# Performance work log

Measured on AMD Instinct MI355X. Metric: run time of the kernel, lower is better.

The kernel has to match this reference:

```python
import jax, jax.numpy as jnp
from jax import lax
import numpy as np

B, T, IN, H, C, L = 128, 80, 4096, 512, 32000, 10


def setup_inputs() -> dict:
    key = jax.random.key(0)
    ks = jax.random.split(key, 19)
    s = 0.05  # param scale for numerical stability
    f = lambda k, shape: (jax.random.normal(k, shape, jnp.float32) * s)
    return {
        "data": jax.random.normal(ks[0], (B, T, IN), jnp.float32),
        "target": jax.random.randint(ks[1], (B, L), 0, C),
        "enc_lin_w": f(ks[2], (H, IN)),
        "enc_lin_b": f(ks[3], (H,)),
        "enc_wih0": f(ks[4], (2, 3 * H, H)),
        "enc_whh0": f(ks[5], (2, 3 * H, H)),
        "enc_bih0": f(ks[6], (2, 3 * H)),
        "enc_bhh0": f(ks[7], (2, 3 * H)),
        "enc_wih1": f(ks[8], (2, 3 * H, 2 * H)),
        "enc_whh1": f(ks[9], (2, 3 * H, H)),
        "enc_bih1": f(ks[10], (2, 3 * H)),
        "enc_bhh1": f(ks[11], (2, 3 * H)),
        "dec_wih": f(ks[12], (3 * H, H)),
        "dec_whh": f(ks[13], (3 * H, H)),
        "dec_bih": f(ks[14], (3 * H,)),
        "dec_bhh": f(ks[15], (3 * H,)),
        "out_w": f(ks[16], (C, 2 * H)),
        "out_b": f(ks[17], (C,)),
        "embed": f(ks[18], (C, H)),
    }


def _gru_cell(x, h, wih, whh, bih, bhh):
    # PyTorch GRU gate math, gates stacked (r, z, n) along 3H.
    gi = x @ wih.T + bih  # (B, 3H)
    gh = h @ whh.T + bhh
    ir, iz, inn = jnp.split(gi, 3, axis=-1)
    hr, hz, hn = jnp.split(gh, 3, axis=-1)
    r = jax.nn.sigmoid(ir + hr)
    z = jax.nn.sigmoid(iz + hz)
    n = jnp.tanh(inn + r * hn)
    return (1.0 - z) * n + z * h


def _gru_layer(x, wih, whh, bih, bhh, reverse):
    # x: (B, T, in) -> outputs (B, T, H), final hidden (B, H)
    h0 = jnp.zeros((x.shape[0], whh.shape[-1]), x.dtype)

    def step(h, xt):
        hn = _gru_cell(xt, h, wih, whh, bih, bhh)
        return hn, hn

    hT, ys = lax.scan(step, h0, jnp.swapaxes(x, 0, 1), reverse=reverse)
    return jnp.swapaxes(ys, 0, 1), hT


def _bidir_layer(x, wih, whh, bih, bhh):
    yf, hf = _gru_layer(x, wih[0], whh[0], bih[0], bhh[0], False)
    yb, hb = _gru_layer(x, wih[1], whh[1], bih[1], bhh[1], True)
    return jnp.concatenate([yf, yb], axis=-1), hf, hb


def reference(data, target, enc_lin_w, enc_lin_b, enc_wih0, enc_whh0, enc_bih0,
              enc_bhh0, enc_wih1, enc_whh1, enc_bih1, enc_bhh1, dec_wih,
              dec_whh, dec_bih, dec_bhh, out_w, out_b, embed):
    # ---- Encoder ----
    x = jax.nn.relu(data @ enc_lin_w.T + enc_lin_b)  # (B, T, H)
    y0, _, _ = _bidir_layer(x, enc_wih0, enc_whh0, enc_bih0, enc_bhh0)
    y1, _, h1b = _bidir_layer(y0, enc_wih1, enc_whh1, enc_bih1, enc_bhh1)
    encode_out = y1[..., :H] + y1[..., H:]  # (B, T, H)
    decode_hid = h1b  # encode_hid[3] = layer-1 backward final hidden (B, H)

    # ---- Decoder loop (teacher forcing; dropout off / eval) ----
    words = target.T  # (L, B)

    def dec_step(h, word):
        emb = embed[word]  # (B, H)
        hn = _gru_cell(emb, h, dec_wih, dec_whh, dec_bih, dec_bhh)
        att = jax.nn.softmax(jnp.einsum('bth,bh->bt', encode_out, hn), axis=1)
        ctx = jnp.einsum('bth,bt->bh', encode_out, att)  # (B, H)
        logits = jnp.concatenate([ctx, hn], axis=-1) @ out_w.T + out_b
        return hn, jax.nn.log_softmax(logits, axis=-1)

    _, logps = lax.scan(dec_step, decode_hid, words)  # (L, B, C)
    pre_prob = jnp.swapaxes(logps, 0, 1)  # (B, L, C)
    pre_sent = jnp.argmax(logps, axis=-1)  # (L, B)
    return pre_prob, pre_sent
```

## Files before the change

### kernel.cpp

```cpp
#include <hip/hip_runtime.h>
#include <cstdint>
#include <cstddef>

#define DEVFN __device__ __forceinline__

DEVFN float sigmf(float x) { return 1.0f / (1.0f + expf(-x)); }

template <int ACT, int RMAP>
__global__ __launch_bounds__(512, 4) void gemm_k(
    const float* __restrict__ A, const float* __restrict__ B,
    const float* __restrict__ bias, float* __restrict__ C, int K, int ldc) {
  constexpr int SST = 132;
  __shared__ float As[2][16 * SST];
  __shared__ float Bs[2][16 * SST];
  const int tid = threadIdx.x;
  const int mA = blockIdx.y * 128;
  const int n0 = blockIdx.x * 128;

  const int sm = tid >> 2;
  const int sq = tid & 3;
  const float* __restrict__ Ap = A + (size_t)(mA + sm) * K + sq * 4;
  const float* __restrict__ Bp = B + (size_t)(n0 + sm) * K + sq * 4;

  const int w = tid >> 6;
  const int lane = tid & 63;
  const int am0 = (w >> 1) * 32 + (lane >> 3) * 4;
  const int bn0 = (w & 1) * 64 + (lane & 7) * 4;

  const float4 fz = {0.f, 0.f, 0.f, 0.f};
  float4 c0a = fz, c0b = fz, c1a = fz, c1b = fz, c2a = fz, c2b = fz,
         c3a = fz, c3b = fz;

#define STAGE_WR(AW, BW, ga, gb)          \
  do {                                    \
    const int kq = sq * 4;                \
    (AW)[(kq + 0) * SST + sm] = (ga).x;   \
    (AW)[(kq + 1) * SST + sm] = (ga).y;   \
    (AW)[(kq + 2) * SST + sm] = (ga).z;   \
    (AW)[(kq + 3) * SST + sm] = (ga).w;   \
    (BW)[(kq + 0) * SST + sm] = (gb).x;   \
    (BW)[(kq + 1) * SST + sm] = (gb).y;   \
    (BW)[(kq + 2) * SST + sm] = (gb).z;   \
    (BW)[(kq + 3) * SST + sm] = (gb).w;   \
  } while (0)

#define FMA8(AV, CA, CB)            \
  CA.x = fmaf(AV, b0.x, CA.x);      \
  CA.y = fmaf(AV, b0.y, CA.y);      \
  CA.z = fmaf(AV, b0.z, CA.z);      \
  CA.w = fmaf(AV, b0.w, CA.w);      \
  CB.x = fmaf(AV, b1.x, CB.x);      \
  CB.y = fmaf(AV, b1.y, CB.y);      \
  CB.z = fmaf(AV, b1.z, CB.z);      \
  CB.w = fmaf(AV, b1.w, CB.w);

#define COMPUTE_TILE(Ab, Bb)                                    \
  _Pragma("unroll") for (int k = 0; k < 16; ++k) {              \
    const float4 av = *(const float4*)&(Ab)[k * SST + am0];     \
    const float4 b0 = *(const float4*)&(Bb)[k * SST + bn0];     \
    const float4 b1 = *(const float4*)&(Bb)[k * SST + bn0 + 32];\
    FMA8(av.x, c0a, c0b)                                        \
    FMA8(av.y, c1a, c1b)                                        \
    FMA8(av.z, c2a, c2b)                                        \
    FMA8(av.w, c3a, c3b)                                        \
  }

  {
    const float4 ga = *(const float4*)Ap;
    const float4 gb = *(const float4*)Bp;
    STAGE_WR(As[0], Bs[0], ga, gb);
  }
  __syncthreads();

  const int nt = K >> 4;
  for (int t = 0; t < nt - 1; ++t) {
    const int kc = (t + 1) << 4;
    const float4 ga = *(const float4*)(Ap + kc);
    const float4 gb = *(const float4*)(Bp + kc);
    const float* __restrict__ Ab = As[t & 1];
    const float* __restrict__ Bb = Bs[t & 1];
    COMPUTE_TILE(Ab, Bb)
    STAGE_WR(As[(t & 1) ^ 1], Bs[(t & 1) ^ 1], ga, gb);
    __syncthreads();
  }
  {
    const float* __restrict__ Ab = As[(nt - 1) & 1];
    const float* __restrict__ Bb = Bs[(nt - 1) & 1];
    COMPUTE_TILE(Ab, Bb)
  }
#undef STAGE_WR
#undef FMA8
#undef COMPUTE_TILE

  const float4 bv0 = *(const float4*)&bias[n0 + bn0];
  const float4 bv1 = *(const float4*)&bias[n0 + bn0 + 32];
#define EPI_ROW(IDX, CA, CB)                                         \
  {                                                                  \
    const int m = mA + am0 + (IDX);                                  \
    int cr;                                                          \
    if (RMAP == 0) cr = m;                                           \
    else if (RMAP == 1) cr = (m % 80) * 128 + m / 80;                \
    else cr = (m & 127) * 10 + (m >> 7);                             \
    float* Cp = C + (size_t)cr * ldc + n0 + bn0;                     \
    float4 o0, o1;                                                   \
    float v;                                                         \
    v = CA.x + bv0.x; o0.x = ACT ? fmaxf(v, 0.f) : v;                \
    v = CA.y + bv0.y; o0.y = ACT ? fmaxf(v, 0.f) : v;                \
    v = CA.z + bv0.z; o0.z = ACT ? fmaxf(v, 0.f) : v;                \
    v = CA.w + bv0.w; o0.w = ACT ? fmaxf(v, 0.f) : v;                \
    v = CB.x + bv1.x; o1.x = ACT ? fmaxf(v, 0.f) : v;                \
    v = CB.y + bv1.y; o1.y = ACT ? fmaxf(v, 0.f) : v;                \
    v = CB.z + bv1.z; o1.z = ACT ? fmaxf(v, 0.f) : v;                \
    v = CB.w + bv1.w; o1.w = ACT ? fmaxf(v, 0.f) : v;                \
    *(float4*)&Cp[0] = o0;                                           \
    *(float4*)&Cp[32] = o1;                                          \
  }
  EPI_ROW(0, c0a, c0b)
  EPI_ROW(1, c1a, c1b)
  EPI_ROW(2, c2a, c2b)
  EPI_ROW(3, c3a, c3b)
#undef EPI_ROW
}

__global__ __launch_bounds__(256, 4) void gru_step_k(
    const float* __restrict__ h_prev, float* __restrict__ h_next,
    const float* __restrict__ gi, int gi_ld, const float* __restrict__ whh,
    const float* __restrict__ bhh, float* __restrict__ y, int y_ld, int i,
    int T) {
  __shared__ float lds_h[16 * 516];
  __shared__ float gh_lds[24 * 17];
  const int tid = threadIdx.x;
  const int jt = blockIdx.x;
  const int bt = blockIdx.y;
  const int d = blockIdx.z;
  const int t_d = (d == 0) ? i : (T - 1 - i);
  const int doff = d * 1536;
  const int j0 = jt * 8;
  const int b0 = bt * 16;

  const int jh2 = tid & 7;
  const int b2g = tid >> 3;
  float g_r = 0.f, g_z = 0.f, g_n = 0.f, bh_r = 0.f, bh_z = 0.f, bh_n = 0.f;
  if (b2g < 16) {
    const float* gir =
        gi + (size_t)(t_d * 128 + b0 + b2g) * gi_ld + doff + j0 + jh2;
    g_r = gir[0];
    g_z = gir[512];
    g_n = gir[1024];
    bh_r = bhh[doff + j0 + jh2];
    bh_z = bhh[doff + 512 + j0 + jh2];
    bh_n = bhh[doff + 1024 + j0 + jh2];
  }

  {
    const float* hp = h_prev + ((size_t)(d * 128 + b0)) * 512;
#pragma unroll
    for (int c = 0; c < 8; ++c) {
      const int i4 = c * 256 + tid;
      const int r = i4 >> 7, k4 = i4 & 127;
      *(float4*)&lds_h[r * 516 + k4 * 4] =
          *(const float4*)&hp[(size_t)r * 512 + k4 * 4];
    }
  }
  __syncthreads();

  const int w = tid >> 6;
  const int lane = tid & 63;
  const int b_loc = lane & 15;
  const int kh = lane >> 4;
  const int kbase = kh * 128;

  const float* wr[6];
#pragma unroll
  for (int q = 0; q < 6; ++q) {
    const int rl = w * 6 + q;
    const int g = rl >> 3, jh = rl & 7;
    wr[q] = whh + ((size_t)(doff + g * 512 + j0 + jh)) * 512 + kbase;
  }
  float acc[6] = {0.f, 0.f, 0.f, 0.f, 0.f, 0.f};
  const float* hrow = &lds_h[b_loc * 516 + kbase];
  for (int k8 = 0; k8 < 128; k8 += 8) {
    const float4 a0 = *(const float4*)&hrow[k8];
    const float4 a1 = *(const float4*)&hrow[k8 + 4];
#pragma unroll
    for (int q = 0; q < 6; ++q) {
      const float* r_ = wr[q] + k8;
      acc[q] += r_[0] * a0.x + r_[1] * a0.y + r_[2] * a0.z + r_[3] * a0.w +
                r_[4] * a1.x + r_[5] * a1.y + r_[6] * a1.z + r_[7] * a1.w;
    }
  }
#pragma unroll
  for (int q = 0; q < 6; ++q) {
    acc[q] += __shfl_xor(acc[q], 16);
    acc[q] += __shfl_xor(acc[q], 32);
  }
  if (kh == 0) {
#pragma unroll
    for (int q = 0; q < 6; ++q) gh_lds[(w * 6 + q) * 17 + b_loc] = acc[q];
  }
  __syncthreads();

  if (b2g < 16) {
    const float ghr = gh_lds[jh2 * 17 + b2g];
    const float ghz = gh_lds[(8 + jh2) * 17 + b2g];
    const float ghn = gh_lds[(16 + jh2) * 17 + b2g];
    const int jg = j0 + jh2;
    const int bg = b0 + b2g;
    const float r = sigmf(g_r + ghr + bh_r);
    const float z = sigmf(g_z + ghz + bh_z);
    const float n = tanhf(g_n + r * (ghn + bh_n));
    const float hold = lds_h[b2g * 516 + jg];
    const float hnew = (1.f - z) * n + z * hold;
    h_next[((size_t)(d * 128 + bg)) * 512 + jg] = hnew;
    y[((size_t)(t_d * 128 + bg)) * y_ld + d * 512 + jg] = hnew;
  }
}

__global__ void fold_k(const float* __restrict__ y1, float* __restrict__ eo) {
  const size_t i = (size_t)blockIdx.x * 256 + threadIdx.x;
  const size_t r = i >> 7;
  const int k4 = (int)(i & 127);
  const float* s = y1 + r * 1024 + k4 * 4;
  const float4 a = *(const float4*)s;
  const float4 c = *(const float4*)(s + 512);
  float4 o;
  o.x = a.x + c.x; o.y = a.y + c.y; o.z = a.z + c.z; o.w = a.w + c.w;
  *(float4*)&eo[r * 512 + k4 * 4] = o;
}

__global__ void gather_k(const float* __restrict__ embed,
                         const int* __restrict__ target,
                         float* __restrict__ out) {
  const int rowid = blockIdx.x;
  const int l = rowid >> 7, b = rowid & 127;
  const int wd = target[b * 10 + l];
  const float4* src = (const float4*)(embed + (size_t)wd * 512);
  float4* dst = (float4*)(out + (size_t)rowid * 512);
  dst[threadIdx.x] = src[threadIdx.x];
}

__global__ __launch_bounds__(256) void attn_k(const float* __restrict__ enc,
                                              const float* __restrict__ hn_all,
                                              float* __restrict__ Z) {
  __shared__ float hs[512];
  __shared__ float sc[80];
  __shared__ float att[80];
  const int l = blockIdx.x >> 7;
  const int b = blockIdx.x & 127;
  const int tid = threadIdx.x;
  const size_t hrow = (size_t)(l * 128 + b) * 512;
  if (tid < 128)
    *(float4*)&hs[tid * 4] = *(const float4*)&hn_all[hrow + tid * 4];
  __syncthreads();
  const int w = tid >> 6, lane = tid & 63;
  for (int t = w; t < 80; t += 4) {
    const float* e = enc + ((size_t)(t * 128 + b)) * 512 + lane * 8;
    const float4 e0 = *(const float4*)e;
    const float4 e1 = *(const float4*)(e + 4);
    const float* h8 = &hs[lane * 8];
    float p = e0.x * h8[0] + e0.y * h8[1] + e0.z * h8[2] + e0.w * h8[3] +
              e1.x * h8[4] + e1.y * h8[5] + e1.z * h8[6] + e1.w * h8[7];
#pragma unroll
    for (int off = 1; off < 64; off <<= 1) p += __shfl_xor(p, off);
    if (lane == 0) sc[t] = p;
  }
  __syncthreads();
  if (w == 0) {
    const float v0 = sc[lane];
    const float v1 = (lane < 16) ? sc[64 + lane] : -3.4e38f;
    float m = fmaxf(v0, v1);
#pragma unroll
    for (int off = 1; off < 64; off <<= 1) m = fmaxf(m, __shfl_xor(m, off));
    const float e0 = expf(v0 - m);
    const float e1 = (lane < 16) ? expf(v1 - m) : 0.f;
    float s = e0 + e1;
#pragma unroll
    for (int off = 1; off < 64; off <<= 1) s += __shfl_xor(s, off);
    att[lane] = e0 / s;
    if (lane < 16) att[64 + lane] = e1 / s;
  }
  __syncthreads();
  float c0 = 0.f, c1 = 0.f;
  for (int t = 0; t < 80; ++t) {
    const float* e = enc + ((size_t)(t * 128 + b)) * 512;
    const float a = att[t];
    c0 += a * e[tid];
    c1 += a * e[tid + 256];
  }
  const size_t zr = (size_t)(l * 128 + b) * 1024;
  Z[zr + tid] = c0;
  Z[zr + 256 + tid] = c1;
  Z[zr + 512 + tid] = hs[tid];
  Z[zr + 768 + tid] = hs[256 + tid];
}

__global__ __launch_bounds__(256) void lsm_k(float* __restrict__ out) {
  const int row = blockIdx.x;
  float* p = out + (size_t)row * 32000;
  const int tid = threadIdx.x;
  float bv = -3.4e38f;
  int bi = 0;
  for (int c = 0; c < 125; ++c) {
    const int idx = c * 256 + tid;
    const float v = p[idx];
    if (v > bv || (v == bv && idx < bi)) { bv = v; bi = idx; }
  }
#pragma unroll
  for (int off = 1; off < 64; off <<= 1) {
    const float ov = __shfl_xor(bv, off);
    const int oi = __shfl_xor(bi, off);
    if (ov > bv || (ov == bv && oi < bi)) { bv = ov; bi = oi; }
  }
  __shared__ float wv[4];
  __shared__ int wi[4];
  __shared__ float wsm[4];
  const int w = tid >> 6, lane = tid & 63;
  if (lane == 0) { wv[w] = bv; wi[w] = bi; }
  __syncthreads();
  float m = wv[0];
  int mi = wi[0];
#pragma unroll
  for (int q = 1; q < 4; ++q) {
    if (wv[q] > m || (wv[q] == m && wi[q] < mi)) { m = wv[q]; mi = wi[q]; }
  }
  float s = 0.f;
  for (int c = 0; c < 125; ++c) s += expf(p[c * 256 + tid] - m);
#pragma unroll
  for (int off = 1; off < 64; off <<= 1) s += __shfl_xor(s, off);
  if (lane == 0) wsm[w] = s;
  __syncthreads();
  const float lse = m + logf(wsm[0] + wsm[1] + wsm[2] + wsm[3]);
  for (int c = 0; c < 125; ++c) {
    const int idx = c * 256 + tid;
    p[idx] = p[idx] - lse;
  }
  if (tid == 0) out[40960000 + (row % 10) * 128 + (row / 10)] = (float)mi;
}

extern "C" void kernel_launch(void* const* d_in, const int* in_sizes, int n_in,
                              void* d_out, int out_size, void* d_ws,
                              size_t ws_size, hipStream_t stream) {
  (void)in_sizes; (void)n_in; (void)out_size; (void)ws_size;
  const float* data = (const float*)d_in[0];
  const int* target = (const int*)d_in[1];
  const float* enc_lin_w = (const float*)d_in[2];
  const float* enc_lin_b = (const float*)d_in[3];
  const float* enc_wih0 = (const float*)d_in[4];
  const float* enc_whh0 = (const float*)d_in[5];
  const float* enc_bih0 = (const float*)d_in[6];
  const float* enc_bhh0 = (const float*)d_in[7];
  const float* enc_wih1 = (const float*)d_in[8];
  const float* enc_whh1 = (const float*)d_in[9];
  const float* enc_bih1 = (const float*)d_in[10];
  const float* enc_bhh1 = (const float*)d_in[11];
  const float* dec_wih = (const float*)d_in[12];
  const float* dec_whh = (const float*)d_in[13];
  const float* dec_bih = (const float*)d_in[14];
  const float* dec_bhh = (const float*)d_in[15];
  const float* out_w = (const float*)d_in[16];
  const float* out_b = (const float*)d_in[17];
  const float* embed = (const float*)d_in[18];
  float* outp = (float*)d_out;

  float* ws = (float*)d_ws;
  size_t off = 0;
  float* buf_gi = ws + off;  off += 31457280;
  float* buf_x = ws + off;   off += 5242880;
  float* buf_y0 = ws + off;  off += 10485760;
  float* buf_y1 = ws + off;  off += 10485760;
  float* h_pp0 = ws + off;   off += 131072;
  float* h_pp1 = ws + off;   off += 131072;
  float* dec_pp0 = ws + off; off += 65536;
  float* dec_pp1 = ws + off; off += 65536;
  float* emb_g = ws + off;   off += 655360;
  float* gi_dec = ws + off;  off += 1966080;
  float* hn_all = ws + off;  off += 655360;
  float* Zb = ws + off;      off += 1310720;

  gemm_k<1, 1><<<dim3(4, 80), 512, 0, stream>>>(data, enc_lin_w, enc_lin_b,
                                                buf_x, 4096, 512);
  gemm_k<0, 0><<<dim3(24, 80), 512, 0, stream>>>(buf_x, enc_wih0, enc_bih0,
                                                 buf_gi, 512, 3072);
  hipMemsetAsync(h_pp0, 0, 2 * 128 * 512 * sizeof(float), stream);
  for (int i = 0; i < 80; ++i) {
    float* hin = (i & 1) ? h_pp1 : h_pp0;
    float* hout = (i & 1) ? h_pp0 : h_pp1;
    gru_step_k<<<dim3(64, 8, 2), 256, 0, stream>>>(
        hin, hout, buf_gi, 3072, enc_whh0, enc_bhh0, buf_y0, 1024, i, 80);
  }
  gemm_k<0, 0><<<dim3(24, 80), 512, 0, stream>>>(buf_y0, enc_wih1, enc_bih1,
                                                 buf_gi, 1024, 3072);
  hipMemsetAsync(h_pp0, 0, 2 * 128 * 512 * sizeof(float), stream);
  for (int i = 0; i < 80; ++i) {
    float* hin = (i & 1) ? h_pp1 : h_pp0;
    float* hout = (i & 1) ? h_pp0 : h_pp1;
    gru_step_k<<<dim3(64, 8, 2), 256, 0, stream>>>(
        hin, hout, buf_gi, 3072, enc_whh1, enc_bhh1, buf_y1, 1024, i, 80);
  }
  fold_k<<<5120, 256, 0, stream>>>(buf_y1, buf_x);
  gather_k<<<1280, 128, 0, stream>>>(embed, target, emb_g);
  gemm_k<0, 0><<<dim3(12, 10), 512, 0, stream>>>(emb_g, dec_wih, dec_bih,
                                                 gi_dec, 512, 1536);
  for (int l = 0; l < 10; ++l) {
    float* hin = (l == 0) ? (h_pp0 + 128 * 512) : ((l & 1) ? dec_pp1 : dec_pp0);
    float* hout = (l & 1) ? dec_pp0 : dec_pp1;
    gru_step_k<<<dim3(64, 8, 1), 256, 0, stream>>>(
        hin, hout, gi_dec, 1536, dec_whh, dec_bhh, hn_all, 512, l, 10);
  }
  attn_k<<<1280, 256, 0, stream>>>(buf_x, hn_all, Zb);
  gemm_k<0, 2><<<dim3(250, 10), 512, 0, stream>>>(Zb, out_w, out_b, outp, 1024,
                                                  32000);
  lsm_k<<<1280, 256, 0, stream>>>(outp);
}
```

Before: 7.654 ms.

## Enlarge GEMM M-tile to 256, reorder output GEMM grid, fuse online softmax

The GEMM kernel now computes a 256x128 output tile per block, with 8 rows by 8 columns of accumulators per thread, doubling A-tile LDS use and register pressure. This raises arithmetic intensity and cuts B-matrix reloads. An MFAST template flag makes M the fast grid dimension for the vocab projection, so blocks sharing an out_w tile run together for L2 reuse. The log-softmax kernel merges the max and sum-exp passes into one online pass over the row, removing one full read of the logits. The larger tile risks lower occupancy and spills under launch_bounds(512,4).

```diff
diff --git a/kernel.cpp b/kernel.cpp
--- a/kernel.cpp
+++ b/kernel.cpp
@@ -6,42 +6,51 @@
 
 DEVFN float sigmf(float x) { return 1.0f / (1.0f + expf(-x)); }
 
-template <int ACT, int RMAP>
+template <int ACT, int RMAP, int MFAST>
 __global__ __launch_bounds__(512, 4) void gemm_k(
     const float* __restrict__ A, const float* __restrict__ B,
     const float* __restrict__ bias, float* __restrict__ C, int K, int ldc) {
-  constexpr int SST = 132;
-  __shared__ float As[2][16 * SST];
-  __shared__ float Bs[2][16 * SST];
+  constexpr int SA = 260;
+  constexpr int SB = 132;
+  __shared__ float As[2][16 * SA];
+  __shared__ float Bs[2][16 * SB];
   const int tid = threadIdx.x;
-  const int mA = blockIdx.y * 128;
-  const int n0 = blockIdx.x * 128;
+  const int mb = MFAST ? blockIdx.x : blockIdx.y;
+  const int nb = MFAST ? blockIdx.y : blockIdx.x;
+  const int mA = mb * 256;
+  const int n0 = nb * 128;
 
   const int sm = tid >> 2;
   const int sq = tid & 3;
-  const float* __restrict__ Ap = A + (size_t)(mA + sm) * K + sq * 4;
+  const float* __restrict__ Ap0 = A + (size_t)(mA + sm) * K + sq * 4;
+  const float* __restrict__ Ap1 = A + (size_t)(mA + sm + 128) * K + sq * 4;
   const float* __restrict__ Bp = B + (size_t)(n0 + sm) * K + sq * 4;
 
   const int w = tid >> 6;
   const int lane = tid & 63;
-  const int am0 = (w >> 1) * 32 + (lane >> 3) * 4;
+  const int am0 = (w >> 1) * 64 + (lane >> 3) * 4;
   const int bn0 = (w & 1) * 64 + (lane & 7) * 4;
 
   const float4 fz = {0.f, 0.f, 0.f, 0.f};
-  float4 c0a = fz, c0b = fz, c1a = fz, c1b = fz, c2a = fz, c2b = fz,
-         c3a = fz, c3b = fz;
-
-#define STAGE_WR(AW, BW, ga, gb)          \
-  do {                                    \
-    const int kq = sq * 4;                \
-    (AW)[(kq + 0) * SST + sm] = (ga).x;   \
-    (AW)[(kq + 1) * SST + sm] = (ga).y;   \
-    (AW)[(kq + 2) * SST + sm] = (ga).z;   \
-    (AW)[(kq + 3) * SST + sm] = (ga).w;   \
-    (BW)[(kq + 0) * SST + sm] = (gb).x;   \
-    (BW)[(kq + 1) * SST + sm] = (gb).y;   \
-    (BW)[(kq + 2) * SST + sm] = (gb).z;   \
-    (BW)[(kq + 3) * SST + sm] = (gb).w;   \
+  float4 r0a = fz, r0b = fz, r1a = fz, r1b = fz, r2a = fz, r2b = fz,
+         r3a = fz, r3b = fz, r4a = fz, r4b = fz, r5a = fz, r5b = fz,
+         r6a = fz, r6b = fz, r7a = fz, r7b = fz;
+
+#define STAGE_WR(AW, BW, ga0, ga1, gb)        \
+  do {                                        \
+    const int kq = sq * 4;                    \
+    (AW)[(kq + 0) * SA + sm] = (ga0).x;       \
+    (AW)[(kq + 1) * SA + sm] = (ga0).y;       \
+    (AW)[(kq + 2) * SA + sm] = (ga0).z;       \
+    (AW)[(kq + 3) * SA + sm] = (ga0).w;       \
+    (AW)[(kq + 0) * SA + sm + 128] = (ga1).x; \
+    (AW)[(kq + 1) * SA + sm + 128] = (ga1).y; \
+    (AW)[(kq + 2) * SA + sm + 128] = (ga1).z; \
+    (AW)[(kq + 3) * SA + sm + 128] = (ga1).w; \
+    (BW)[(kq + 0) * SB + sm] = (gb).x;        \
+    (BW)[(kq + 1) * SB + sm] = (gb).y;        \
+    (BW)[(kq + 2) * SB + sm] = (gb).z;        \
+    (BW)[(kq + 3) * SB + sm] = (gb).w;        \
   } while (0)
 
 #define FMA8(AV, CA, CB)            \
@@ -54,33 +63,40 @@
   CB.z = fmaf(AV, b1.z, CB.z);      \
   CB.w = fmaf(AV, b1.w, CB.w);
 
-#define COMPUTE_TILE(Ab, Bb)                                    \
-  _Pragma("unroll") for (int k = 0; k < 16; ++k) {              \
-    const float4 av = *(const float4*)&(Ab)[k * SST + am0];     \
-    const float4 b0 = *(const float4*)&(Bb)[k * SST + bn0];     \
-    const float4 b1 = *(const float4*)&(Bb)[k * SST + bn0 + 32];\
-    FMA8(av.x, c0a, c0b)                                        \
-    FMA8(av.y, c1a, c1b)                                        \
-    FMA8(av.z, c2a, c2b)                                        \
-    FMA8(av.w, c3a, c3b)                                        \
+#define COMPUTE_TILE(Ab, Bb)                                     \
+  _Pragma("unroll") for (int k = 0; k < 16; ++k) {               \
+    const float4 a0 = *(const float4*)&(Ab)[k * SA + am0];       \
+    const float4 a1 = *(const float4*)&(Ab)[k * SA + am0 + 32];  \
+    const float4 b0 = *(const float4*)&(Bb)[k * SB + bn0];       \
+    const float4 b1 = *(const float4*)&(Bb)[k * SB + bn0 + 32];  \
+    FMA8(a0.x, r0a, r0b)                                         \
+    FMA8(a0.y, r1a, r1b)                                         \
+    FMA8(a0.z, r2a, r2b)                                         \
+    FMA8(a0.w, r3a, r3b)                                         \
+    FMA8(a1.x, r4a, r4b)                                         \
+    FMA8(a1.y, r5a, r5b)                                         \
+    FMA8(a1.z, r6a, r6b)                                         \
+    FMA8(a1.w, r7a, r7b)                                         \
   }
 
   {
-    const float4 ga = *(const float4*)Ap;
+    const float4 ga0 = *(const float4*)Ap0;
+    const float4 ga1 = *(const float4*)Ap1;
     const float4 gb = *(const float4*)Bp;
-    STAGE_WR(As[0], Bs[0], ga, gb);
+    STAGE_WR(As[0], Bs[0], ga0, ga1, gb);
   }
   __syncthreads();
 
   const int nt = K >> 4;
   for (int t = 0; t < nt - 1; ++t) {
     const int kc = (t + 1) << 4;
-    const float4 ga = *(const float4*)(Ap + kc);
+    const float4 ga0 = *(const float4*)(Ap0 + kc);
+    const float4 ga1 = *(const float4*)(Ap1 + kc);
     const float4 gb = *(const float4*)(Bp + kc);
     const float* __restrict__ Ab = As[t & 1];
     const float* __restrict__ Bb = Bs[t & 1];
     COMPUTE_TILE(Ab, Bb)
-    STAGE_WR(As[(t & 1) ^ 1], Bs[(t & 1) ^ 1], ga, gb);
+    STAGE_WR(As[(t & 1) ^ 1], Bs[(t & 1) ^ 1], ga0, ga1, gb);
     __syncthreads();
   }
   {
@@ -96,7 +112,7 @@
   const float4 bv1 = *(const float4*)&bias[n0 + bn0 + 32];
 #define EPI_ROW(IDX, CA, CB)                                         \
   {                                                                  \
-    const int m = mA + am0 + (IDX);                                  \
+    const int m = mA + am0 + ((IDX) < 4 ? (IDX) : 28 + (IDX));       \
     int cr;                                                          \
     if (RMAP == 0) cr = m;                                           \
     else if (RMAP == 1) cr = (m % 80) * 128 + m / 80;                \
@@ -115,10 +131,14 @@
     *(float4*)&Cp[0] = o0;                                           \
     *(float4*)&Cp[32] = o1;                                          \
   }
-  EPI_ROW(0, c0a, c0b)
-  EPI_ROW(1, c1a, c1b)
-  EPI_ROW(2, c2a, c2b)
-  EPI_ROW(3, c3a, c3b)
+  EPI_ROW(0, r0a, r0b)
+  EPI_ROW(1, r1a, r1b)
+  EPI_ROW(2, r2a, r2b)
+  EPI_ROW(3, r3a, r3b)
+  EPI_ROW(4, r4a, r4b)
+  EPI_ROW(5, r5a, r5b)
+  EPI_ROW(6, r6a, r6b)
+  EPI_ROW(7, r7a, r7b)
 #undef EPI_ROW
 }
 
@@ -298,43 +318,64 @@
   const int row = blockIdx.x;
   float* p = out + (size_t)row * 32000;
   const int tid = threadIdx.x;
-  float bv = -3.4e38f;
+  float m = -3.4e38f, s = 0.f;
   int bi = 0;
   for (int c = 0; c < 125; ++c) {
     const int idx = c * 256 + tid;
     const float v = p[idx];
-    if (v > bv || (v == bv && idx < bi)) { bv = v; bi = idx; }
+    if (v > m) {
+      s = s * expf(m - v) + 1.f;
+      m = v;
+      bi = idx;
+    } else {
+      s += expf(v - m);
+    }
   }
 #pragma unroll
   for (int off = 1; off < 64; off <<= 1) {
-    const float ov = __shfl_xor(bv, off);
+    const float om = __shfl_xor(m, off);
+    const float os = __shfl_xor(s, off);
     const int oi = __shfl_xor(bi, off);
-    if (ov > bv || (ov == bv && oi < bi)) { bv = ov; bi = oi; }
-  }
-  __shared__ float wv[4];
+    if (om > m) {
+      s = s * expf(m - om) + os;
+      m = om;
+      bi = oi;
+    } else if (om == m) {
+      s += os;
+      bi = (oi < bi) ? oi : bi;
+    } else {
+      s += os * expf(om - m);
+    }
+  }
+  __shared__ float wm[4];
+  __shared__ float wsm[4];
   __shared__ int wi[4];
-  __shared__ float wsm[4];
   const int w = tid >> 6, lane = tid & 63;
-  if (lane == 0) { wv[w] = bv; wi[w] = bi; }
-  __syncthreads();
-  float m = wv[0];
-  int mi = wi[0];
+  if (lane == 0) { wm[w] = m; wsm[w] = s; wi[w] = bi; }
+  __syncthreads();
+  float M = wm[0], S = wsm[0];
+  int MI = wi[0];
 #pragma unroll
   for (int q = 1; q < 4; ++q) {
-    if (wv[q] > m || (wv[q] == m && wi[q] < mi)) { m = wv[q]; mi = wi[q]; }
-  }
-  float s = 0.f;
-  for (int c = 0; c < 125; ++c) s += expf(p[c * 256 + tid] - m);
-#pragma unroll
-  for (int off = 1; off < 64; off <<= 1) s += __shfl_xor(s, off);
-  if (lane == 0) wsm[w] = s;
-  __syncthreads();
-  const float lse = m + logf(wsm[0] + wsm[1] + wsm[2] + wsm[3]);
+    const float om = wm[q], os = wsm[q];
+    const int oi = wi[q];
+    if (om > M) {
+      S = S * expf(M - om) + os;
+      M = om;
+      MI = oi;
+    } else if (om == M) {
+      S += os;
+      MI = (oi < MI) ? oi : MI;
+    } else {
+      S += os * expf(om - M);
+    }
+  }
+  const float lse = M + logf(S);
   for (int c = 0; c < 125; ++c) {
     const int idx = c * 256 + tid;
     p[idx] = p[idx] - lse;
   }
-  if (tid == 0) out[40960000 + (row % 10) * 128 + (row / 10)] = (float)mi;
+  if (tid == 0) out[40960000 + (row % 10) * 128 + (row / 10)] = (float)MI;
 }
 
 extern "C" void kernel_launch(void* const* d_in, const int* in_sizes, int n_in,
@@ -377,10 +418,10 @@
   float* hn_all = ws + off;  off += 655360;
   float* Zb = ws + off;      off += 1310720;
 
-  gemm_k<1, 1><<<dim3(4, 80), 512, 0, stream>>>(data, enc_lin_w, enc_lin_b,
-                                                buf_x, 4096, 512);
-  gemm_k<0, 0><<<dim3(24, 80), 512, 0, stream>>>(buf_x, enc_wih0, enc_bih0,
-                                                 buf_gi, 512, 3072);
+  gemm_k<1, 1, 0><<<dim3(4, 40), 512, 0, stream>>>(data, enc_lin_w, enc_lin_b,
+                                                   buf_x, 4096, 512);
+  gemm_k<0, 0, 0><<<dim3(24, 40), 512, 0, stream>>>(buf_x, enc_wih0, enc_bih0,
+                                                    buf_gi, 512, 3072);
   hipMemsetAsync(h_pp0, 0, 2 * 128 * 512 * sizeof(float), stream);
   for (int i = 0; i < 80; ++i) {
     float* hin = (i & 1) ? h_pp1 : h_pp0;
@@ -388,8 +429,9 @@
     gru_step_k<<<dim3(64, 8, 2), 256, 0, stream>>>(
         hin, hout, buf_gi, 3072, enc_whh0, enc_bhh0, buf_y0, 1024, i, 80);
   }
-  gemm_k<0, 0><<<dim3(24, 80), 512, 0, stream>>>(buf_y0, enc_wih1, enc_bih1,
-                                                 buf_gi, 1024, 3072);
+  gemm_k<0, 0, 0><<<dim3(24, 40), 512, 0, stream>>>(buf_y0, enc_wih1,
+                                                    enc_bih1, buf_gi, 1024,
+                                                    3072);
   hipMemsetAsync(h_pp0, 0, 2 * 128 * 512 * sizeof(float), stream);
   for (int i = 0; i < 80; ++i) {
     float* hin = (i & 1) ? h_pp1 : h_pp0;
@@ -399,8 +441,8 @@
   }
   fold_k<<<5120, 256, 0, stream>>>(buf_y1, buf_x);
   gather_k<<<1280, 128, 0, stream>>>(embed, target, emb_g);
-  gemm_k<0, 0><<<dim3(12, 10), 512, 0, stream>>>(emb_g, dec_wih, dec_bih,
-                                                 gi_dec, 512, 1536);
+  gemm_k<0, 0, 0><<<dim3(12, 5), 512, 0, stream>>>(emb_g, dec_wih, dec_bih,
+                                                   gi_dec, 512, 1536);
   for (int l = 0; l < 10; ++l) {
     float* hin = (l == 0) ? (h_pp0 + 128 * 512) : ((l & 1) ? dec_pp1 : dec_pp0);
     float* hout = (l & 1) ? dec_pp0 : dec_pp1;
@@ -408,7 +450,7 @@
         hin, hout, gi_dec, 1536, dec_whh, dec_bhh, hn_all, 512, l, 10);
   }
   attn_k<<<1280, 256, 0, stream>>>(buf_x, hn_all, Zb);
-  gemm_k<0, 2><<<dim3(250, 10), 512, 0, stream>>>(Zb, out_w, out_b, outp, 1024,
-                                                  32000);
+  gemm_k<0, 2, 1><<<dim3(5, 250), 512, 0, stream>>>(Zb, out_w, out_b, outp,
+                                                    1024, 32000);
   lsm_k<<<1280, 256, 0, stream>>>(outp);
 }
```

Result: slower. 8.374 ms (+9.4%).
